# Optimization experiments

Measured on AMD Instinct MI355X. Metric: run time of the kernel, lower is better.

## Reference

```python
import jax, jax.numpy as jnp
import numpy as np

D_MODEL = 1024
NUM_HEADS = 16
D_HEAD = D_MODEL // NUM_HEADS
B, T_Q, T_K = 2, 2048, 2048


def setup_inputs() -> dict:
    key = jax.random.key(0)
    ks = jax.random.split(key, 7)
    s = 0.02
    return {
        "query": jax.random.normal(ks[0], (B, T_Q, D_MODEL), jnp.float32),
        "key_value": jax.random.normal(ks[1], (B, T_K, D_MODEL), jnp.float32),
        "mask": jax.random.randint(ks[2], (B, 1, T_Q, T_K), 0, 2, jnp.int32),
        "rel_pos_bias": jax.random.normal(ks[3], (NUM_HEADS, T_Q, T_K), jnp.float32),
        "Wq": jax.random.normal(ks[4], (D_MODEL, D_MODEL), jnp.float32) * s,
        "Wkv": jax.random.normal(ks[5], (D_MODEL, 2 * D_MODEL), jnp.float32) * s,
        "Wo": jax.random.normal(ks[6], (D_MODEL, D_MODEL), jnp.float32) * s,
    }


def reference(query, key_value, mask, rel_pos_bias, Wq, Wkv, Wo):
    Bq, Tq, D = query.shape
    Tk = key_value.shape[1]
    H, Dh = NUM_HEADS, D_HEAD
    q = (query @ Wq).reshape(Bq, Tq, H, Dh)              # [B,Tq,H,Dh]
    kv = (key_value @ Wkv).reshape(Bq, Tk, 2, H, Dh)
    k, v = kv[:, :, 0], kv[:, :, 1]                      # [B,Tk,H,Dh]
    scale = 1.0 / jnp.sqrt(jnp.asarray(Dh, q.dtype))
    scores = jnp.einsum("bqhd,bkhd->bhqk", q, k) * scale  # [B,H,Tq,Tk]
    scores = scores + rel_pos_bias[None]                  # bias broadcast over batch
    scores = jnp.where(mask == 0, -jnp.inf, scores)
    attn = jax.nn.softmax(scores, axis=-1)
    out = jnp.einsum("bhqk,bkhd->bqhd", attn, v).reshape(Bq, Tq, D)
    return out @ Wo
```

## Files before the change

kernel.cpp:

```cpp
#include <hip/hip_runtime.h>

typedef unsigned short u16;
typedef unsigned int u32;
typedef unsigned long long u64;
typedef __attribute__((ext_vector_type(4))) float f32x4;
typedef __attribute__((ext_vector_type(4))) unsigned short u16x4;
typedef __attribute__((ext_vector_type(8))) short short8;

#define GLOAD16(G, L) __builtin_amdgcn_global_load_lds( \
    (const __attribute__((address_space(1))) void*)(G), \
    (__attribute__((address_space(3))) void*)(L), 16, 0, 0)

__device__ __forceinline__ u16 f2bf(float f) {
  union { float f; unsigned u; } c; c.f = f;
  unsigned u = c.u;
  u += 0x7FFFu + ((u >> 16) & 1u);
  return (u16)(u >> 16);
}

__device__ __forceinline__ void store_out(u16* p, float v) { *p = f2bf(v); }
__device__ __forceinline__ void store_out(float* p, float v) { *p = v; }

__global__ void k_cvt(const float* __restrict__ in, u16* __restrict__ out, int n4) {
  int i = blockIdx.x * blockDim.x + threadIdx.x;
  if (i >= n4) return;
  const f32x4 v = *(const f32x4*)(in + (size_t)i * 4);
  u16x4 o;
  o[0] = f2bf(v[0]); o[1] = f2bf(v[1]); o[2] = f2bf(v[2]); o[3] = f2bf(v[3]);
  *(u16x4*)(out + (size_t)i * 4) = o;
}

__global__ void k_tcvt(const float* __restrict__ src, u16* __restrict__ dst,
                       int R, int C, float scale) {
  __shared__ float t[32][33];
  int bx = blockIdx.x * 32;
  int by = blockIdx.y * 32;
  int tx = threadIdx.x, ty = threadIdx.y;
  #pragma unroll
  for (int j = 0; j < 32; j += 8)
    t[ty + j][tx] = src[(size_t)(by + ty + j) * C + bx + tx];
  __syncthreads();
  #pragma unroll
  for (int j = 0; j < 32; j += 8)
    dst[(size_t)(bx + ty + j) * R + by + tx] = f2bf(t[tx][ty + j] * scale);
}

__global__ void k_tv(const u16* __restrict__ kv, u16* __restrict__ vt) {
  __shared__ u16 sh[32][34];
  int b = blockIdx.z;
  int tb = blockIdx.x * 32;
  int db = blockIdx.y * 32;
  int tx = threadIdx.x, ty = threadIdx.y;
  #pragma unroll
  for (int j = 0; j < 32; j += 8)
    sh[ty + j][tx] = kv[(size_t)(b * 2048 + tb + ty + j) * 2048 + 1024 + db + tx];
  __syncthreads();
  int t = tb + tx;
  int k6 = t & 63;
  int colp = (t & ~63) | (((k6 >> 2) & 3) << 4) | ((k6 >> 4) << 2) | (k6 & 3);
  #pragma unroll
  for (int j = 0; j < 32; j += 8)
    vt[(size_t)(b * 1024 + db + ty + j) * 2048 + colp] = sh[tx][ty + j];
}

__global__ void k_pm(const int* __restrict__ mask, unsigned* __restrict__ bits, int nw) {
  int w = blockIdx.x * blockDim.x + threadIdx.x;
  if (w >= nw) return;
  const int4* p = (const int4*)(mask + (size_t)w * 32);
  unsigned b = 0;
  #pragma unroll
  for (int j = 0; j < 8; ++j) {
    int4 v = p[j];
    b |= (v.x != 0 ? 1u : 0u) << (j * 4);
    b |= (v.y != 0 ? 1u : 0u) << (j * 4 + 1);
    b |= (v.z != 0 ? 1u : 0u) << (j * 4 + 2);
    b |= (v.w != 0 ? 1u : 0u) << (j * 4 + 3);
  }
  bits[w] = b;
}

template <int BM, int BN, typename OUT_T>
__global__ __launch_bounds__(256) void k_gemm(
    const u16* __restrict__ A, const u16* __restrict__ Bt,
    OUT_T* __restrict__ C, int M, int N, int K)
{
  constexpr int MI = BM / 32, NI = BN / 32;
  __shared__ u16 As[BM * 64];
  __shared__ u16 Bs[BN * 64];
  const int tid = threadIdx.x;
  const int lane = tid & 63;
  const int w = tid >> 6;
  const int wr = w >> 1, wc = w & 1;
  const int l16 = lane & 15, lh = lane >> 4;
  const size_t tm = blockIdx.x, tn = blockIdx.y;

  f32x4 acc[MI][NI] = {};

  for (int kt = 0; kt < K; kt += 64) {
    #pragma unroll
    for (int i = 0; i < BM / 32; ++i) {
      int flat = i * 256 + tid;
      int row = flat >> 3, cb = flat & 7;
      GLOAD16(A + (tm * BM + row) * K + kt + ((cb ^ (row & 7)) * 8),
              (char*)As + flat * 16);
    }
    #pragma unroll
    for (int i = 0; i < BN / 32; ++i) {
      int flat = i * 256 + tid;
      int row = flat >> 3, cb = flat & 7;
      GLOAD16(Bt + (tn * BN + row) * K + kt + ((cb ^ (row & 7)) * 8),
              (char*)Bs + flat * 16);
    }
    __syncthreads();
    #pragma unroll
    for (int kk = 0; kk < 2; ++kk) {
      short8 a[MI], b[NI];
      #pragma unroll
      for (int mi = 0; mi < MI; ++mi) {
        int row = wr * (BM / 2) + mi * 16 + l16;
        a[mi] = *(const short8*)&As[row * 64 + ((kk * 32 + lh * 8) ^ ((row & 7) * 8))];
      }
      #pragma unroll
      for (int ni = 0; ni < NI; ++ni) {
        int row = wc * (BN / 2) + ni * 16 + l16;
        b[ni] = *(const short8*)&Bs[row * 64 + ((kk * 32 + lh * 8) ^ ((row & 7) * 8))];
      }
      #pragma unroll
      for (int mi = 0; mi < MI; ++mi)
        #pragma unroll
        for (int ni = 0; ni < NI; ++ni)
          acc[mi][ni] = __builtin_amdgcn_mfma_f32_16x16x32_bf16(a[mi], b[ni], acc[mi][ni], 0, 0, 0);
    }
    __syncthreads();
  }
  #pragma unroll
  for (int mi = 0; mi < MI; ++mi)
    #pragma unroll
    for (int ni = 0; ni < NI; ++ni)
      #pragma unroll
      for (int r = 0; r < 4; ++r) {
        size_t row = tm * BM + wr * (BM / 2) + mi * 16 + lh * 4 + r;
        size_t col = tn * BN + wc * (BN / 2) + ni * 16 + l16;
        store_out(&C[row * N + col], acc[mi][ni][r]);
      }
}

__global__ __launch_bounds__(512, 4) void k_attn(
    const u16* __restrict__ Qp,
    const u16* __restrict__ KVp,
    const u16* __restrict__ Vt,
    const float* __restrict__ bias,
    const unsigned* __restrict__ mbits,
    u16* __restrict__ Ob)
{
  __shared__ u16 Ks[2 * 2 * 64 * 64];
  __shared__ u16 Vs[2 * 2 * 64 * 64];
  const int tid = threadIdx.x;
  const int lane = tid & 63;
  const int w = tid >> 6;
  const int bw = w >> 2;
  const int qs = (w & 3) * 16;
  const int qt = blockIdx.x;
  const int h  = blockIdx.y;
  const int l16 = lane & 15, lh = lane >> 4;
  const int q = qt * 64 + qs + l16;

  const int srow = tid >> 3, scb = tid & 7;
  const u16* ksrc = KVp + (size_t)srow * 2048 + h * 64 + ((scb ^ (srow & 7)) * 8);
  const u16* vsrc = Vt + ((size_t)(h * 64 + srow)) * 2048 + ((scb ^ (srow & 7)) * 8);

  short8 qf[2];
  {
    size_t row = (size_t)bw * 2048 + q;
    qf[0] = *(const short8*)&Qp[row * 1024 + h * 64 + lh * 8];
    qf[1] = *(const short8*)&Qp[row * 1024 + h * 64 + 32 + lh * 8];
  }

  const float* bsrc = bias + ((size_t)h * 2048 + q) * 2048 + lh * 4;
  const u64*   msrc = (const u64*)(mbits + ((size_t)bw * 2048 + q) * 64);

  f32x4 oacc[4] = {};
  f32x4 lpv = {};
  f32x4 biasA[4], biasB[4];
  u64 mwA, mwB;

  GLOAD16(ksrc,                       &Ks[tid * 8]);
  GLOAD16(ksrc + (size_t)2048 * 2048, &Ks[4096 + tid * 8]);
  GLOAD16(vsrc,                       &Vs[tid * 8]);
  GLOAD16(vsrc + (size_t)1024 * 2048, &Vs[4096 + tid * 8]);
  #pragma unroll
  for (int ni = 0; ni < 4; ++ni) {
    biasA[ni] = *(const f32x4*)(bsrc + ni * 16);
    biasB[ni] = *(const f32x4*)(bsrc + 64 + ni * 16);
  }
  mwA = msrc[0];
  mwB = msrc[1];
  asm volatile("s_waitcnt vmcnt(0)" ::: "memory");
  __builtin_amdgcn_s_barrier();

#define ASTEP(KT, CUR, BC, MC) do {                                                     \
    const int ktp1_ = ((KT) + 1 < 32) ? (KT) + 1 : 31;                                  \
    const int ktp2_ = ((KT) + 2 < 32) ? (KT) + 2 : 31;                                  \
    const int nb_ = (CUR) ^ 1;                                                          \
    GLOAD16(ksrc + (size_t)ktp1_ * 64 * 2048,                  &Ks[nb_ * 8192 + tid * 8]);        \
    GLOAD16(ksrc + ((size_t)2048 + (size_t)ktp1_ * 64) * 2048, &Ks[nb_ * 8192 + 4096 + tid * 8]); \
    GLOAD16(vsrc + (size_t)ktp1_ * 64,                         &Vs[nb_ * 8192 + tid * 8]);        \
    GLOAD16(vsrc + (size_t)1024 * 2048 + (size_t)ktp1_ * 64,   &Vs[nb_ * 8192 + 4096 + tid * 8]); \
    __builtin_amdgcn_sched_barrier(0);                                                  \
    f32x4 s_[4];                                                                        \
    s_[0] = BC[0]; s_[1] = BC[1]; s_[2] = BC[2]; s_[3] = BC[3];                         \
    const unsigned tlo_ = (unsigned)(MC) >> (lh * 4);                                   \
    const unsigned thi_ = (unsigned)((MC) >> 32) >> (lh * 4);                           \
    BC[0] = *(const f32x4*)(bsrc + (size_t)ktp2_ * 64 +  0);                            \
    BC[1] = *(const f32x4*)(bsrc + (size_t)ktp2_ * 64 + 16);                            \
    BC[2] = *(const f32x4*)(bsrc + (size_t)ktp2_ * 64 + 32);                            \
    BC[3] = *(const f32x4*)(bsrc + (size_t)ktp2_ * 64 + 48);                            \
    MC = msrc[ktp2_];                                                                   \
    const int kb_ = (CUR) * 8192 + bw * 4096;                                           \
    __builtin_amdgcn_s_setprio(1);                                                      \
    _Pragma("unroll")                                                                   \
    for (int kk = 0; kk < 2; ++kk) {                                                    \
      short8 kf_[4];                                                                    \
      _Pragma("unroll")                                                                 \
      for (int ni = 0; ni < 4; ++ni) {                                                  \
        const int row_ = ni * 16 + l16;                                                 \
        kf_[ni] = *(const short8*)&Ks[kb_ + row_ * 64 + ((kk * 32 + lh * 8) ^ ((row_ & 7) * 8))]; \
      }                                                                                 \
      _Pragma("unroll")                                                                 \
      for (int ni = 0; ni < 4; ++ni)                                                    \
        s_[ni] = __builtin_amdgcn_mfma_f32_16x16x32_bf16(kf_[ni], qf[kk], s_[ni], 0, 0, 0); \
    }                                                                                   \
    __builtin_amdgcn_s_setprio(0);                                                      \
    union pfu_ { u32 wd[4]; short8 v; };                                                \
    union pfu_ pf_[2];                                                                  \
    _Pragma("unroll")                                                                   \
    for (int ni = 0; ni < 4; ++ni) {                                                    \
      const unsigned tw_ = (ni < 2) ? tlo_ : thi_;                                      \
      _Pragma("unroll")                                                                 \
      for (int r = 0; r < 4; ++r) {                                                     \
        const unsigned bit_ = (tw_ >> ((ni & 1) * 16 + r)) & 1u;                        \
        s_[ni][r] = bit_ ? __expf(s_[ni][r]) : 0.f;                                     \
      }                                                                                 \
      lpv += s_[ni];                                                                    \
      asm("v_cvt_pk_bf16_f32 %0, %1, %2" : "=v"(pf_[ni >> 1].wd[2 * (ni & 1)])     : "v"(s_[ni][0]), "v"(s_[ni][1])); \
      asm("v_cvt_pk_bf16_f32 %0, %1, %2" : "=v"(pf_[ni >> 1].wd[2 * (ni & 1) + 1]) : "v"(s_[ni][2]), "v"(s_[ni][3])); \
    }                                                                                   \
    __builtin_amdgcn_s_setprio(1);                                                      \
    _Pragma("unroll")                                                                   \
    for (int kk = 0; kk < 2; ++kk) {                                                    \
      _Pragma("unroll")                                                                 \
      for (int di = 0; di < 4; ++di) {                                                  \
        const int row_ = di * 16 + l16;                                                 \
        short8 vf_ = *(const short8*)&Vs[kb_ + row_ * 64 + (((lh * 2 + kk) * 8) ^ ((row_ & 7) * 8))]; \
        oacc[di] = __builtin_amdgcn_mfma_f32_16x16x32_bf16(vf_, pf_[kk].v, oacc[di], 0, 0, 0); \
      }                                                                                 \
    }                                                                                   \
    __builtin_amdgcn_s_setprio(0);                                                      \
    asm volatile("s_waitcnt lgkmcnt(0)" ::: "memory");                                  \
    asm volatile("s_waitcnt vmcnt(5)" ::: "memory");                                    \
    __builtin_amdgcn_s_barrier();                                                       \
  } while (0)

  for (int kt2 = 0; kt2 < 32; kt2 += 2) {
    ASTEP(kt2,     0, biasA, mwA);
    ASTEP(kt2 + 1, 1, biasB, mwB);
  }
#undef ASTEP

  float lpart = lpv[0] + lpv[1] + lpv[2] + lpv[3];
  lpart += __shfl_xor(lpart, 16);
  lpart += __shfl_xor(lpart, 32);
  float inv = 1.0f / lpart;
  size_t orow = (size_t)bw * 2048 + q;
  #pragma unroll
  for (int di = 0; di < 4; ++di)
    #pragma unroll
    for (int rp = 0; rp < 2; ++rp) {
      float v0 = oacc[di][2 * rp] * inv;
      float v1 = oacc[di][2 * rp + 1] * inv;
      u32 pk;
      asm("v_cvt_pk_bf16_f32 %0, %1, %2" : "=v"(pk) : "v"(v0), "v"(v1));
      *(u32*)&Ob[orow * 1024 + h * 64 + di * 16 + lh * 4 + rp * 2] = pk;
    }
}

extern "C" void kernel_launch(void* const* d_in, const int* in_sizes, int n_in,
                              void* d_out, int out_size, void* d_ws, size_t ws_size,
                              hipStream_t stream) {
  const float* query     = (const float*)d_in[0];
  const float* key_value = (const float*)d_in[1];
  const int*   mask      = (const int*)d_in[2];
  const float* bias      = (const float*)d_in[3];
  const float* Wq        = (const float*)d_in[4];
  const float* Wkv       = (const float*)d_in[5];
  const float* Wo        = (const float*)d_in[6];
  float* out = (float*)d_out;

  char* ws = (char*)d_ws;
  u16* qb   = (u16*)(ws);
  u16* kvb  = (u16*)(ws + 8388608);
  u16* WqT  = (u16*)(ws + 16777216);
  u16* WkvT = (u16*)(ws + 18874368);
  u16* WoT  = (u16*)(ws + 23068672);
  u16* Qp   = (u16*)(ws + 25165824);
  u16* KVp  = (u16*)(ws + 33554432);
  u16* Vt   = (u16*)(ws + 50331648);
  u16* Ob   = (u16*)(ws + 58720256);
  unsigned* mb = (unsigned*)(ws + 67108864);

  dim3 tb(32, 8);
  k_cvt<<<4096, 256, 0, stream>>>(query, qb, 1048576);
  k_cvt<<<4096, 256, 0, stream>>>(key_value, kvb, 1048576);
  k_tcvt<<<dim3(32, 32), tb, 0, stream>>>(Wq,  WqT,  1024, 1024, 0.125f);
  k_tcvt<<<dim3(64, 32), tb, 0, stream>>>(Wkv, WkvT, 1024, 2048, 1.0f);
  k_tcvt<<<dim3(32, 32), tb, 0, stream>>>(Wo,  WoT,  1024, 1024, 1.0f);
  k_pm<<<1024, 256, 0, stream>>>(mask, mb, 262144);
  k_gemm<64, 128, u16><<<dim3(64, 8),  256, 0, stream>>>(qb,  WqT,  Qp,  4096, 1024, 1024);
  k_gemm<64, 128, u16><<<dim3(64, 16), 256, 0, stream>>>(kvb, WkvT, KVp, 4096, 2048, 1024);
  k_tv<<<dim3(64, 32, 2), tb, 0, stream>>>(KVp, Vt);
  k_attn<<<dim3(32, 16), 512, 0, stream>>>(Qp, KVp, Vt, bias, mb, Ob);
  k_gemm<64, 128, float><<<dim3(64, 8), 256, 0, stream>>>(Ob, WoT, out, 4096, 1024, 1024);
}
```

Measured before the change: 232.7 us.

## Load K/V fragments directly from global into registers, drop LDS staging

The attention kernel drops the shared-memory double buffer and barriers. Each wave now loads its K and V MFMA fragments straight from global memory into registers, with K prefetched two tiles ahead. Blocks shrink to 256 threads handling 4 independent 16-query waves, and the 1D grid uses a swizzled block-to-(head,batch,qtile) mapping so co-resident blocks share K/V through L2. This removes LDS traffic and sync, but each wave re-reads K/V from cache rather than sharing it within the block. It also raises register pressure.

```diff
diff --git a/kernel.cpp b/kernel.cpp
--- a/kernel.cpp
+++ b/kernel.cpp
@@ -145,7 +145,7 @@
       }
 }
 
-__global__ __launch_bounds__(512, 4) void k_attn(
+__global__ __launch_bounds__(256, 2) void k_attn(
     const u16* __restrict__ Qp,
     const u16* __restrict__ KVp,
     const u16* __restrict__ Vt,
@@ -153,84 +153,72 @@
     const unsigned* __restrict__ mbits,
     u16* __restrict__ Ob)
 {
-  __shared__ u16 Ks[2 * 2 * 64 * 64];
-  __shared__ u16 Vs[2 * 2 * 64 * 64];
   const int tid = threadIdx.x;
   const int lane = tid & 63;
   const int w = tid >> 6;
-  const int bw = w >> 2;
-  const int qs = (w & 3) * 16;
-  const int qt = blockIdx.x;
-  const int h  = blockIdx.y;
+  const int bid = blockIdx.x;
+  const int sid = (bid & 7) * 128 + (bid >> 3);
+  const int h  = sid >> 6;
+  const int bw = (sid >> 5) & 1;
+  const int qt = (sid & 31) * 4 + w;
   const int l16 = lane & 15, lh = lane >> 4;
-  const int q = qt * 64 + qs + l16;
-
-  const int srow = tid >> 3, scb = tid & 7;
-  const u16* ksrc = KVp + (size_t)srow * 2048 + h * 64 + ((scb ^ (srow & 7)) * 8);
-  const u16* vsrc = Vt + ((size_t)(h * 64 + srow)) * 2048 + ((scb ^ (srow & 7)) * 8);
-
-  short8 qf[2];
+  const int q = qt * 16 + l16;
+
+  const u16* kfp = KVp + ((size_t)bw * 2048 + l16) * 2048 + h * 64 + lh * 8;
+  const u16* vfp = Vt + ((size_t)(bw * 1024 + h * 64 + l16)) * 2048 + lh * 16;
+
+  short8 qf0, qf1;
   {
     size_t row = (size_t)bw * 2048 + q;
-    qf[0] = *(const short8*)&Qp[row * 1024 + h * 64 + lh * 8];
-    qf[1] = *(const short8*)&Qp[row * 1024 + h * 64 + 32 + lh * 8];
+    qf0 = *(const short8*)&Qp[row * 1024 + h * 64 + lh * 8];
+    qf1 = *(const short8*)&Qp[row * 1024 + h * 64 + 32 + lh * 8];
   }
-
   const float* bsrc = bias + ((size_t)h * 2048 + q) * 2048 + lh * 4;
   const u64*   msrc = (const u64*)(mbits + ((size_t)bw * 2048 + q) * 64);
 
   f32x4 oacc[4] = {};
   f32x4 lpv = {};
-  f32x4 biasA[4], biasB[4];
-  u64 mwA, mwB;
-
-  GLOAD16(ksrc,                       &Ks[tid * 8]);
-  GLOAD16(ksrc + (size_t)2048 * 2048, &Ks[4096 + tid * 8]);
-  GLOAD16(vsrc,                       &Vs[tid * 8]);
-  GLOAD16(vsrc + (size_t)1024 * 2048, &Vs[4096 + tid * 8]);
-  #pragma unroll
-  for (int ni = 0; ni < 4; ++ni) {
-    biasA[ni] = *(const f32x4*)(bsrc + ni * 16);
-    biasB[ni] = *(const f32x4*)(bsrc + 64 + ni * 16);
-  }
-  mwA = msrc[0];
-  mwB = msrc[1];
-  asm volatile("s_waitcnt vmcnt(0)" ::: "memory");
-  __builtin_amdgcn_s_barrier();
-
-#define ASTEP(KT, CUR, BC, MC) do {                                                     \
-    const int ktp1_ = ((KT) + 1 < 32) ? (KT) + 1 : 31;                                  \
-    const int ktp2_ = ((KT) + 2 < 32) ? (KT) + 2 : 31;                                  \
-    const int nb_ = (CUR) ^ 1;                                                          \
-    GLOAD16(ksrc + (size_t)ktp1_ * 64 * 2048,                  &Ks[nb_ * 8192 + tid * 8]);        \
-    GLOAD16(ksrc + ((size_t)2048 + (size_t)ktp1_ * 64) * 2048, &Ks[nb_ * 8192 + 4096 + tid * 8]); \
-    GLOAD16(vsrc + (size_t)ktp1_ * 64,                         &Vs[nb_ * 8192 + tid * 8]);        \
-    GLOAD16(vsrc + (size_t)1024 * 2048 + (size_t)ktp1_ * 64,   &Vs[nb_ * 8192 + 4096 + tid * 8]); \
-    __builtin_amdgcn_sched_barrier(0);                                                  \
+  short8 kA[8], kB[8];
+  f32x4 bA[4], bB[4];
+  u64 mA, mB;
+
+#define LOADSET(KC, BC, MC, KT) do {                                                    \
+    _Pragma("unroll")                                                                   \
+    for (int ni_ = 0; ni_ < 4; ++ni_) {                                                 \
+      _Pragma("unroll")                                                                 \
+      for (int kk_ = 0; kk_ < 2; ++kk_)                                                 \
+        KC[ni_ * 2 + kk_] = *(const short8*)(kfp + ((size_t)((KT) * 64 + ni_ * 16)) * 2048 + kk_ * 32); \
+      BC[ni_] = *(const f32x4*)(bsrc + (size_t)(KT) * 64 + ni_ * 16);                   \
+    }                                                                                   \
+    MC = msrc[(KT)];                                                                    \
+  } while (0)
+
+  LOADSET(kA, bA, mA, 0);
+  LOADSET(kB, bB, mB, 1);
+
+#define STEP(KT, KC, BC, MC) do {                                                       \
     f32x4 s_[4];                                                                        \
     s_[0] = BC[0]; s_[1] = BC[1]; s_[2] = BC[2]; s_[3] = BC[3];                         \
     const unsigned tlo_ = (unsigned)(MC) >> (lh * 4);                                   \
     const unsigned thi_ = (unsigned)((MC) >> 32) >> (lh * 4);                           \
-    BC[0] = *(const f32x4*)(bsrc + (size_t)ktp2_ * 64 +  0);                            \
-    BC[1] = *(const f32x4*)(bsrc + (size_t)ktp2_ * 64 + 16);                            \
-    BC[2] = *(const f32x4*)(bsrc + (size_t)ktp2_ * 64 + 32);                            \
-    BC[3] = *(const f32x4*)(bsrc + (size_t)ktp2_ * 64 + 48);                            \
-    MC = msrc[ktp2_];                                                                   \
-    const int kb_ = (CUR) * 8192 + bw * 4096;                                           \
-    __builtin_amdgcn_s_setprio(1);                                                      \
-    _Pragma("unroll")                                                                   \
-    for (int kk = 0; kk < 2; ++kk) {                                                    \
-      short8 kf_[4];                                                                    \
-      _Pragma("unroll")                                                                 \
-      for (int ni = 0; ni < 4; ++ni) {                                                  \
-        const int row_ = ni * 16 + l16;                                                 \
-        kf_[ni] = *(const short8*)&Ks[kb_ + row_ * 64 + ((kk * 32 + lh * 8) ^ ((row_ & 7) * 8))]; \
-      }                                                                                 \
+    _Pragma("unroll")                                                                   \
+    for (int kk = 0; kk < 2; ++kk)                                                      \
       _Pragma("unroll")                                                                 \
       for (int ni = 0; ni < 4; ++ni)                                                    \
-        s_[ni] = __builtin_amdgcn_mfma_f32_16x16x32_bf16(kf_[ni], qf[kk], s_[ni], 0, 0, 0); \
+        s_[ni] = __builtin_amdgcn_mfma_f32_16x16x32_bf16(KC[ni * 2 + kk],               \
+                     (kk ? qf1 : qf0), s_[ni], 0, 0, 0);                                \
+                     \
+    short8 vf_[8];                                                                      \
+    _Pragma("unroll")                                                                   \
+    for (int di = 0; di < 4; ++di)                                                      \
+      _Pragma("unroll")                                                                 \
+      for (int kk = 0; kk < 2; ++kk)                                                    \
+        vf_[di * 2 + kk] = *(const short8*)(vfp + (size_t)di * 16 * 2048 + (size_t)(KT) * 64 + kk * 8); \
+                                      \
+    {                                                                                   \
+      const int ktn_ = ((KT) + 2 < 32) ? (KT) + 2 : 31;                                 \
+      LOADSET(KC, BC, MC, ktn_);                                                        \
     }                                                                                   \
-    __builtin_amdgcn_s_setprio(0);                                                      \
     union pfu_ { u32 wd[4]; short8 v; };                                                \
     union pfu_ pf_[2];                                                                  \
     _Pragma("unroll")                                                                   \
@@ -245,27 +233,19 @@
       asm("v_cvt_pk_bf16_f32 %0, %1, %2" : "=v"(pf_[ni >> 1].wd[2 * (ni & 1)])     : "v"(s_[ni][0]), "v"(s_[ni][1])); \
       asm("v_cvt_pk_bf16_f32 %0, %1, %2" : "=v"(pf_[ni >> 1].wd[2 * (ni & 1) + 1]) : "v"(s_[ni][2]), "v"(s_[ni][3])); \
     }                                                                                   \
-    __builtin_amdgcn_s_setprio(1);                                                      \
-    _Pragma("unroll")                                                                   \
-    for (int kk = 0; kk < 2; ++kk) {                                                    \
-      _Pragma("unroll")                                                                 \
-      for (int di = 0; di < 4; ++di) {                                                  \
-        const int row_ = di * 16 + l16;                                                 \
-        short8 vf_ = *(const short8*)&Vs[kb_ + row_ * 64 + (((lh * 2 + kk) * 8) ^ ((row_ & 7) * 8))]; \
-        oacc[di] = __builtin_amdgcn_mfma_f32_16x16x32_bf16(vf_, pf_[kk].v, oacc[di], 0, 0, 0); \
-      }                                                                                 \
-    }                                                                                   \
-    __builtin_amdgcn_s_setprio(0);                                                      \
-    asm volatile("s_waitcnt lgkmcnt(0)" ::: "memory");                                  \
-    asm volatile("s_waitcnt vmcnt(5)" ::: "memory");                                    \
-    __builtin_amdgcn_s_barrier();                                                       \
+    _Pragma("unroll")                                                                   \
+    for (int kk = 0; kk < 2; ++kk)                                                      \
+      _Pragma("unroll")                                                                 \
+      for (int di = 0; di < 4; ++di)                                                    \
+        oacc[di] = __builtin_amdgcn_mfma_f32_16x16x32_bf16(vf_[di * 2 + kk], pf_[kk].v, oacc[di], 0, 0, 0); \
   } while (0)
 
-  for (int kt2 = 0; kt2 < 32; kt2 += 2) {
-    ASTEP(kt2,     0, biasA, mwA);
-    ASTEP(kt2 + 1, 1, biasB, mwB);
+  for (int kt = 0; kt < 32; kt += 2) {
+    STEP(kt,     kA, bA, mA);
+    STEP(kt + 1, kB, bB, mB);
   }
-#undef ASTEP
+#undef STEP
+#undef LOADSET
 
   float lpart = lpv[0] + lpv[1] + lpv[2] + lpv[3];
   lpart += __shfl_xor(lpart, 16);
@@ -318,6 +298,6 @@
   k_gemm<64, 128, u16><<<dim3(64, 8),  256, 0, stream>>>(qb,  WqT,  Qp,  4096, 1024, 1024);
   k_gemm<64, 128, u16><<<dim3(64, 16), 256, 0, stream>>>(kvb, WkvT, KVp, 4096, 2048, 1024);
   k_tv<<<dim3(64, 32, 2), tb, 0, stream>>>(KVp, Vt);
-  k_attn<<<dim3(32, 16), 512, 0, stream>>>(Qp, KVp, Vt, bias, mb, Ob);
+  k_attn<<<1024, 256, 0, stream>>>(Qp, KVp, Vt, bias, mb, Ob);
   k_gemm<64, 128, float><<<dim3(64, 8), 256, 0, stream>>>(Ob, WoT, out, 4096, 1024, 1024);
 }
```

Result: slower. 413.2 us (+77.6%).
